# Kernel optimization log

Hardware: AMD Instinct MI355X
Metric: run time of the kernel (lower is better)

The kernel has to match this reference:

```python
import jax, jax.numpy as jnp
import numpy as np

N = 524288
H = 128
EPS = 1e-4
SYMP_N = 32  # min(N, 32)
# loss weights from init_kwargs
W_RECON, W_CONS, W_EVO, W_SYMP, W_GAUGE = 1.0, 10.0, 5.0, 0.1, 5.0


def _mlp(x, W1, b1, W2, b2, W3, b3):
    h = jnp.tanh(x @ W1 + b1)
    h = jnp.tanh(h @ W2 + b2)
    return h @ W3 + b3


def _encode(p, q, params):
    out = _mlp(jnp.stack([p, q], axis=-1), *params)  # [N,2]
    return out[:, 0], out[:, 1]


def _decode(P, Q, params):
    out = _mlp(jnp.stack([P, Q], axis=-1), *params)
    return out[:, 0], out[:, 1]


def setup_inputs() -> dict:
    key = jax.random.key(0)
    ks = jax.random.split(key, 24)
    f32 = jnp.float32

    def nrm(k, shape, scale=1.0):
        return (scale * jax.random.normal(k, shape, dtype=f32))

    inp = {
        'p0': nrm(ks[0], (N,)),
        'q0': nrm(ks[1], (N,)),
        'p1': nrm(ks[2], (N,)),
        'q1': nrm(ks[3], (N,)),
        'omega_values': jax.random.uniform(ks[4], (N,), dtype=f32, minval=0.5, maxval=2.0),
        'dt': jnp.asarray(0.05, dtype=f32),
        'P_true': nrm(ks[5], (N,)),
        'Q_true': nrm(ks[6], (N,)),
        # encoder params (2 -> H -> H -> 2), fan-in scaled init
        'enc_W1': nrm(ks[7], (2, H), 1.0 / np.sqrt(2.0)),
        'enc_b1': jnp.zeros((H,), f32),
        'enc_W2': nrm(ks[8], (H, H), 1.0 / np.sqrt(H)),
        'enc_b2': jnp.zeros((H,), f32),
        'enc_W3': nrm(ks[9], (H, 2), 1.0 / np.sqrt(H)),
        'enc_b3': jnp.zeros((2,), f32),
        # decoder params
        'dec_W1': nrm(ks[10], (2, H), 1.0 / np.sqrt(2.0)),
        'dec_b1': jnp.zeros((H,), f32),
        'dec_W2': nrm(ks[11], (H, H), 1.0 / np.sqrt(H)),
        'dec_b2': jnp.zeros((H,), f32),
        'dec_W3': nrm(ks[12], (H, 2), 1.0 / np.sqrt(H)),
        'dec_b3': jnp.zeros((2,), f32),
    }
    return inp


def _loss(p0, q0, p1, q1, omega_values, dt, P_true, Q_true, enc, dec):
    P0, Q0 = _encode(p0, q0, enc)
    P1, Q1 = _encode(p1, q1, enc)
    p0_recon, q0_recon = _decode(P0, Q0, dec)

    recon_loss = jnp.mean((p0 - p0_recon) ** 2 + (q0 - q0_recon) ** 2)
    conservation_loss = jnp.mean((P0 - P1) ** 2)
    evolution_loss = jnp.mean(1.0 - jnp.cos((Q1 - Q0) - omega_values * dt))

    # symplectic loss: batched central finite differences over first 32 samples
    pi, qi = p0[:SYMP_N], q0[:SYMP_N]
    pp = jnp.concatenate([pi + EPS, pi - EPS, pi, pi])          # [4*32]
    qq = jnp.concatenate([qi, qi, qi + EPS, qi - EPS])
    P, Q = _encode(pp, qq, enc)
    P_pp, P_pm, P_qp, P_qm = jnp.split(P, 4)
    Q_pp, Q_pm, Q_qp, Q_qm = jnp.split(Q, 4)
    inv2e = 1.0 / (2.0 * EPS)
    dP_dp = (P_pp - P_pm) * inv2e
    dP_dq = (P_qp - P_qm) * inv2e
    dQ_dp = (Q_pp - Q_pm) * inv2e
    dQ_dq = (Q_qp - Q_qm) * inv2e
    pb = dP_dq * dQ_dp - dP_dp * dQ_dq
    symplectic_loss = jnp.mean((jnp.abs(pb) - 1.0) ** 2)

    gauge_loss = jnp.mean((P0 - P_true) ** 2) + jnp.mean(1.0 - jnp.cos(Q0 - Q_true))

    total = (W_RECON * recon_loss + W_CONS * conservation_loss
             + W_EVO * evolution_loss + W_SYMP * symplectic_loss
             + W_GAUGE * gauge_loss)
    return jnp.stack([total, recon_loss, conservation_loss,
                      evolution_loss, symplectic_loss, gauge_loss])


def reference(p0, q0, p1, q1, omega_values, dt, P_true, Q_true,
              enc_W1, enc_b1, enc_W2, enc_b2, enc_W3, enc_b3,
              dec_W1, dec_b1, dec_W2, dec_b2, dec_W3, dec_b3):
    enc = (enc_W1, enc_b1, enc_W2, enc_b2, enc_W3, enc_b3)
    dec = (dec_W1, dec_b1, dec_W2, dec_b2, dec_W3, dec_b3)
    return _loss(p0, q0, p1, q1, omega_values, dt, P_true, Q_true, enc, dec)
```

## Files before the change

### kernel.cpp

```cpp
#include <hip/hip_runtime.h>
#include <stdint.h>
#include <math.h>


constexpr float EPS_FD = 1e-4f;
constexpr int NBLK = 256;

typedef float f32x4 __attribute__((ext_vector_type(4)));
typedef short s16x8 __attribute__((ext_vector_type(8)));

__device__ __forceinline__ float tanh_fast(float x) {
  float e = __builtin_amdgcn_exp2f(x * 2.8853900817779268f);
  return 1.0f - 2.0f * __builtin_amdgcn_rcpf(e + 1.0f);
}
__device__ __forceinline__ float cos_fast(float x) {
  return __builtin_amdgcn_cosf(x * 0.15915494309189535f);
}
__device__ __forceinline__ unsigned bf16rne(float f) {
  union { float f; unsigned u; } v; v.f = f;
  return (v.u + 0x7FFFu + ((v.u >> 16) & 1u)) >> 16;
}
__device__ __forceinline__ unsigned pack2rne(float a, float b) {
  return bf16rne(a) | (bf16rne(b) << 16);
}
__device__ __forceinline__ unsigned packbf(float lo, float hi) {
  union { float f; unsigned u; } a, b; a.f = lo; b.f = hi;
  return __builtin_amdgcn_perm(b.u + 0x8000u, a.u + 0x8000u, 0x07060302u);
}

__global__ void setup_kernel(const float* __restrict__ encW2,
                             const float* __restrict__ decW2,
                             unsigned* __restrict__ frag,
                             const float* __restrict__ p0, const float* __restrict__ q0,
                             const float* __restrict__ W1, const float* __restrict__ b1,
                             const float* __restrict__ W2, const float* __restrict__ b2,
                             const float* __restrict__ W3, const float* __restrict__ b3,
                             float* __restrict__ PQ,
                             float* __restrict__ acc5, unsigned* __restrict__ counter)
{
  int tid = threadIdx.x;
  if (blockIdx.x < 64) {
    if (blockIdx.x == 0 && tid < 6) {
      if (tid < 5) acc5[tid] = 0.f; else *counter = 0u;
    }
    int id = blockIdx.x * 256 + tid;
    const float* W = (id < 8192) ? encW2 : decW2;
    int l = id & 8191;
    int jj   = l & 3;
    int lane = (l >> 2) & 63;
    int f    = l >> 8;
    int s = f >> 3, t = f & 7;
    int quad = lane >> 4, nn = lane & 15;
    int k   = 32 * s + quad * 8 + 2 * jj;
    int col = 16 * t + nn;
    frag[id] = pack2rne(W[k * 128 + col], W[(k + 1) * 128 + col]);
  } else {
    int half = tid >> 7;
    int tt   = tid & 127;
    int row  = (blockIdx.x - 64) * 2 + half;
    int m = row & 31, c = row >> 5;
    float p = p0[m], q = q0[m];
    if (c == 0) p += EPS_FD; else if (c == 1) p -= EPS_FD;
    else if (c == 2) q += EPS_FD; else q -= EPS_FD;

    __shared__ float h1[2][128];
    h1[half][tt] = tanhf(fmaf(p, W1[tt], fmaf(q, W1[128 + tt], b1[tt])));
    __syncthreads();
    float a = b2[tt];
    for (int k = 0; k < 128; k++) a = fmaf(h1[half][k], W2[k * 128 + tt], a);
    float hh = tanhf(a);
    float cP = hh * W3[2 * tt];
    float cQ = hh * W3[2 * tt + 1];
#pragma unroll
    for (int mm = 1; mm < 64; mm <<= 1) {
      cP += __shfl_xor(cP, mm, 64);
      cQ += __shfl_xor(cQ, mm, 64);
    }
    __shared__ float rr[4][2];
    int wv = tid >> 6, ln = tid & 63;
    if (ln == 0) { rr[wv][0] = cP; rr[wv][1] = cQ; }
    __syncthreads();
    if (tt == 0) {
      PQ[2 * row]     = rr[2 * half][0] + rr[2 * half + 1][0] + b3[0];
      PQ[2 * row + 1] = rr[2 * half][1] + rr[2 * half + 1][1] + b3[1];
    }
  }
}

template<bool SCAT, bool EPI_LDS>
__device__ __forceinline__ void mlp_pass(
    float pe, float qe, unsigned* hrow, const uint4* Bf,
    float w100, float w101, float w110, float w111, float b10, float b11,
    const float (&rb2)[8], const float (&rw3P)[8], const float (&rw3Q)[8],
    const float* epi,
    int lane, int quad, int l15, float b3P, float b3Q,
    float& vP, float& vQ)
{
#pragma unroll
  for (int ee = 0; ee < 16; ee++) {
    int src = SCAT ? (16 * (ee >> 2) + (ee & 3)) : ee;
    float p = __shfl(pe, src, 64);
    float q = __shfl(qe, src, 64);
    float a0 = tanh_fast(fmaf(p, w100, fmaf(q, w110, b10)));
    float a1 = tanh_fast(fmaf(p, w101, fmaf(q, w111, b11)));
    hrow[ee * 68 + lane] = packbf(a0, a1);
  }
  __builtin_amdgcn_wave_barrier();

  s16x8 A[4];
#pragma unroll
  for (int s = 0; s < 4; s++) {
    uint4 u = *reinterpret_cast<const uint4*>(&hrow[l15 * 68 + 16 * s + 4 * quad]);
    A[s] = *reinterpret_cast<s16x8*>(&u);
  }
  __builtin_amdgcn_wave_barrier();

  float b2v[8];
#pragma unroll
  for (int t = 0; t < 8; t++) b2v[t] = EPI_LDS ? epi[16 * t + l15] : rb2[t];

  f32x4 acc[8];
#pragma unroll
  for (int t = 0; t < 8; t++) {
    f32x4 z = {b2v[t], b2v[t], b2v[t], b2v[t]};
    acc[t] = z;
  }
#pragma unroll
  for (int s = 0; s < 4; s++) {
#pragma unroll
    for (int t = 0; t < 8; t++) {
      uint4 bu = Bf[(s * 8 + t) * 64 + lane];
      s16x8 Bv = *reinterpret_cast<s16x8*>(&bu);
      acc[t] = __builtin_amdgcn_mfma_f32_16x16x32_bf16(A[s], Bv, acc[t], 0, 0, 0);
    }
  }

  float w3Pv[8], w3Qv[8];
#pragma unroll
  for (int t = 0; t < 8; t++) {
    w3Pv[t] = EPI_LDS ? epi[128 + 16 * t + l15] : rw3P[t];
    w3Qv[t] = EPI_LDS ? epi[256 + 16 * t + l15] : rw3Q[t];
  }

  float sP[4] = {0, 0, 0, 0}, sQ[4] = {0, 0, 0, 0};
#pragma unroll
  for (int t = 0; t < 8; t++) {
#pragma unroll
    for (int r = 0; r < 4; r++) {
      float h = tanh_fast(acc[t][r]);
      sP[r] = fmaf(h, w3Pv[t], sP[r]);
      sQ[r] = fmaf(h, w3Qv[t], sQ[r]);
    }
  }
#pragma unroll
  for (int m = 1; m < 16; m <<= 1) {
#pragma unroll
    for (int r = 0; r < 4; r++) {
      sP[r] += __shfl_xor(sP[r], m, 64);
      sQ[r] += __shfl_xor(sQ[r], m, 64);
    }
  }
  vP = ((l15 == 0) ? sP[0] : (l15 == 1) ? sP[1] : (l15 == 2) ? sP[2] : sP[3]) + b3P;
  vQ = ((l15 == 0) ? sQ[0] : (l15 == 1) ? sQ[1] : (l15 == 2) ? sQ[2] : sQ[3]) + b3Q;
}

__global__ __launch_bounds__(1024, 4) void mlp_all(
    const float* __restrict__ p0, const float* __restrict__ q0,
    const float* __restrict__ p1, const float* __restrict__ q1,
    const uint4* __restrict__ w2frag,
    const float* __restrict__ eW1, const float* __restrict__ eb1,
    const float* __restrict__ eb2, const float* __restrict__ eW3,
    const float* __restrict__ eb3,
    const float* __restrict__ dW1, const float* __restrict__ db1,
    const float* __restrict__ db2, const float* __restrict__ dW3,
    const float* __restrict__ db3,
    const float* __restrict__ omega, const float* __restrict__ Pt,
    const float* __restrict__ Qt, const float* __restrict__ dtp,
    float* __restrict__ acc5, unsigned* __restrict__ counter,
    const float* __restrict__ PQ, float* __restrict__ out, int n)
{
  __shared__ uint4 BfE[2048];
  __shared__ uint4 BfD[2048];
  __shared__ unsigned h1s[16][16 * 68 + 4];
  __shared__ float decEpi[384];
  __shared__ float red[16][5];
  __shared__ unsigned lastflag;

  int tid = threadIdx.x;
  for (int i = tid; i < 2048; i += 1024) {
    BfE[i] = w2frag[i];
    BfD[i] = w2frag[2048 + i];
  }
  if (tid < 128) {
    decEpi[tid]       = db2[tid];
    decEpi[128 + tid] = dW3[2 * tid];
    decEpi[256 + tid] = dW3[2 * tid + 1];
  }

  int wave = tid >> 6, lane = tid & 63;
  int quad = lane >> 4, l15 = lane & 15;

  float ew100 = eW1[2 * lane],       ew101 = eW1[2 * lane + 1];
  float ew110 = eW1[128 + 2 * lane], ew111 = eW1[128 + 2 * lane + 1];
  float eb10 = eb1[2 * lane], eb11 = eb1[2 * lane + 1];
  float dw100 = dW1[2 * lane],       dw101 = dW1[2 * lane + 1];
  float dw110 = dW1[128 + 2 * lane], dw111 = dW1[128 + 2 * lane + 1];
  float db10 = db1[2 * lane], db11 = db1[2 * lane + 1];
  float eb2v[8], ew3P[8], ew3Q[8];
#pragma unroll
  for (int t = 0; t < 8; t++) {
    eb2v[t] = eb2[16 * t + l15];
    ew3P[t] = eW3[(16 * t + l15) * 2];
    ew3Q[t] = eW3[(16 * t + l15) * 2 + 1];
  }
  float eb3P = eb3[0], eb3Q = eb3[1];
  float db3P = db3[0], db3Q = db3[1];
  float dt = dtp[0];
  float s0 = 0.f, s1 = 0.f, s2 = 0.f, s3 = 0.f, s4 = 0.f;
  __syncthreads();

  int nwaves = gridDim.x * 16;
  int gwave  = blockIdx.x * 16 + wave;
  int ntiles = (n + 15) >> 4;
  unsigned* hrow = &h1s[wave][0];

  for (int tile = gwave; tile < ntiles; tile += nwaves) {
    int base = tile * 16;
    int e = base + l15; if (e >= n) e = n - 1;
    float p0e = p0[e], q0e = q0[e];
    float p1e = p1[e], q1e = q1[e];
    int o = base + quad * 4 + l15;
    int o16 = base + quad * 4 + (l15 & 3);
    if (o16 >= n) o16 = n - 1;
    float Lom = omega[o16], LPt = Pt[o16], LQt = Qt[o16];
    float Lp0 = p0[o16],    Lq0 = q0[o16];

    float P0v, Q0v, P1v, Q1v, RPv, RQv;
    mlp_pass<false, false>(p0e, q0e, hrow, BfE,
                           ew100, ew101, ew110, ew111, eb10, eb11,
                           eb2v, ew3P, ew3Q, decEpi,
                           lane, quad, l15, eb3P, eb3Q, P0v, Q0v);
    mlp_pass<false, false>(p1e, q1e, hrow, BfE,
                           ew100, ew101, ew110, ew111, eb10, eb11,
                           eb2v, ew3P, ew3Q, decEpi,
                           lane, quad, l15, eb3P, eb3Q, P1v, Q1v);
    mlp_pass<true, true>(P0v, Q0v, hrow, BfD,
                         dw100, dw101, dw110, dw111, db10, db11,
                         eb2v, ew3P, ew3Q, decEpi,
                         lane, quad, l15, db3P, db3Q, RPv, RQv);

    if (l15 < 4 && o < n) {
      float dp = Lp0 - RPv, dq = Lq0 - RQv;
      s0 += dp * dp + dq * dq;
      float d1 = P0v - P1v; s1 += d1 * d1;
      s2 += 1.0f - cos_fast(Q1v - Q0v - Lom * dt);
      float g = P0v - LPt; s3 += g * g;
      s4 += 1.0f - cos_fast(Q0v - LQt);
    }
  }

#pragma unroll
  for (int m = 1; m < 64; m <<= 1) {
    s0 += __shfl_xor(s0, m, 64);
    s1 += __shfl_xor(s1, m, 64);
    s2 += __shfl_xor(s2, m, 64);
    s3 += __shfl_xor(s3, m, 64);
    s4 += __shfl_xor(s4, m, 64);
  }
  if (lane == 0) {
    red[wave][0] = s0; red[wave][1] = s1; red[wave][2] = s2;
    red[wave][3] = s3; red[wave][4] = s4;
  }
  __syncthreads();
  if (tid == 0) {
#pragma unroll
    for (int i = 0; i < 5; i++) {
      float v = 0.f;
#pragma unroll
      for (int w = 0; w < 16; w++) v += red[w][i];
      atomicAdd(&acc5[i], v);
    }
    __threadfence();
    unsigned prev = atomicAdd(counter, 1u);
    lastflag = (prev == gridDim.x - 1) ? 1u : 0u;
  }
  __syncthreads();
  if (lastflag) {
    __threadfence();
    if (tid < 64) {
      float v = 0.f;
      if (tid < 32) {
        float Ppp = PQ[2 * tid],          Qpp = PQ[2 * tid + 1];
        float Ppm = PQ[2 * (32 + tid)],   Qpm = PQ[2 * (32 + tid) + 1];
        float Pqp = PQ[2 * (64 + tid)],   Qqp = PQ[2 * (64 + tid) + 1];
        float Pqm = PQ[2 * (96 + tid)],   Qqm = PQ[2 * (96 + tid) + 1];
        float inv2e = 1.0f / (2.0f * EPS_FD);
        float dPdp = (Ppp - Ppm) * inv2e, dPdq = (Pqp - Pqm) * inv2e;
        float dQdp = (Qpp - Qpm) * inv2e, dQdq = (Qqp - Qqm) * inv2e;
        float pb = dPdq * dQdp - dPdp * dQdq;
        float d = fabsf(pb) - 1.0f;
        v = d * d;
      }
#pragma unroll
      for (int m = 1; m < 64; m <<= 1) v += __shfl_xor(v, m, 64);
      if (tid == 0) {
        float inv_n = 1.0f / (float)n;
        float recon = atomicAdd(&acc5[0], 0.f) * inv_n;
        float cons  = atomicAdd(&acc5[1], 0.f) * inv_n;
        float evo   = atomicAdd(&acc5[2], 0.f) * inv_n;
        float gauge = (atomicAdd(&acc5[3], 0.f) + atomicAdd(&acc5[4], 0.f)) * inv_n;
        float symp  = v * (1.0f / 32.0f);
        float total = recon + 10.0f * cons + 5.0f * evo + 0.1f * symp + 5.0f * gauge;
        out[0] = total; out[1] = recon; out[2] = cons;
        out[3] = evo;   out[4] = symp;  out[5] = gauge;
      }
    }
  }
}

extern "C" void kernel_launch(void* const* d_in, const int* in_sizes, int n_in,
                              void* d_out, int out_size, void* d_ws, size_t ws_size,
                              hipStream_t stream)
{
  const float* p0    = (const float*)d_in[0];
  const float* q0    = (const float*)d_in[1];
  const float* p1    = (const float*)d_in[2];
  const float* q1    = (const float*)d_in[3];
  const float* omega = (const float*)d_in[4];
  const float* dtp   = (const float*)d_in[5];
  const float* Pt    = (const float*)d_in[6];
  const float* Qt    = (const float*)d_in[7];
  const float* encW1 = (const float*)d_in[8];
  const float* encb1 = (const float*)d_in[9];
  const float* encW2 = (const float*)d_in[10];
  const float* encb2 = (const float*)d_in[11];
  const float* encW3 = (const float*)d_in[12];
  const float* encb3 = (const float*)d_in[13];
  const float* decW1 = (const float*)d_in[14];
  const float* decb1 = (const float*)d_in[15];
  const float* decW2 = (const float*)d_in[16];
  const float* decb2 = (const float*)d_in[17];
  const float* decW3 = (const float*)d_in[18];
  const float* decb3 = (const float*)d_in[19];

  int n = in_sizes[0];
  char* ws = (char*)d_ws;
  unsigned* frag = (unsigned*)ws;
  float* PQ   = (float*)(ws + 65536);
  float* acc5 = PQ + 256;
  unsigned* counter = (unsigned*)(acc5 + 8);

  setup_kernel<<<128, 256, 0, stream>>>(encW2, decW2, frag,
                                        p0, q0, encW1, encb1, encW2, encb2,
                                        encW3, encb3, PQ, acc5, counter);

  mlp_all<<<NBLK, 1024, 0, stream>>>(
      p0, q0, p1, q1, (const uint4*)frag,
      encW1, encb1, encb2, encW3, encb3,
      decW1, decb1, decb2, decW3, decb3,
      omega, Pt, Qt, dtp,
      acc5, counter, PQ, (float*)d_out, n);
}
```

Measured before the change: 293.0 us.

## Restructure launch: pack W2 fragments in-kernel, move symplectic FD and finalize to tail kernel

Removes the separate setup kernel: each main block now converts encoder/decoder W2 into bf16 MFMA fragments directly in LDS, and encoder epilogue weights move from registers to LDS. The last-block atomic counter finalization is replaced by a single-block tail kernel that computes the 32-sample finite-difference symplectic loss and the final output, plus a memset for the accumulators. The aim is to cut the serial setup stage and the counter handshake. In exchange every block redundantly reads and packs 2x64KB of weights, and the small tail kernel runs after the main one, adding its own latency.

```diff
diff --git a/kernel.cpp b/kernel.cpp
--- a/kernel.cpp
+++ b/kernel.cpp
@@ -28,73 +28,11 @@
   return __builtin_amdgcn_perm(b.u + 0x8000u, a.u + 0x8000u, 0x07060302u);
 }
 
-__global__ void setup_kernel(const float* __restrict__ encW2,
-                             const float* __restrict__ decW2,
-                             unsigned* __restrict__ frag,
-                             const float* __restrict__ p0, const float* __restrict__ q0,
-                             const float* __restrict__ W1, const float* __restrict__ b1,
-                             const float* __restrict__ W2, const float* __restrict__ b2,
-                             const float* __restrict__ W3, const float* __restrict__ b3,
-                             float* __restrict__ PQ,
-                             float* __restrict__ acc5, unsigned* __restrict__ counter)
-{
-  int tid = threadIdx.x;
-  if (blockIdx.x < 64) {
-    if (blockIdx.x == 0 && tid < 6) {
-      if (tid < 5) acc5[tid] = 0.f; else *counter = 0u;
-    }
-    int id = blockIdx.x * 256 + tid;
-    const float* W = (id < 8192) ? encW2 : decW2;
-    int l = id & 8191;
-    int jj   = l & 3;
-    int lane = (l >> 2) & 63;
-    int f    = l >> 8;
-    int s = f >> 3, t = f & 7;
-    int quad = lane >> 4, nn = lane & 15;
-    int k   = 32 * s + quad * 8 + 2 * jj;
-    int col = 16 * t + nn;
-    frag[id] = pack2rne(W[k * 128 + col], W[(k + 1) * 128 + col]);
-  } else {
-    int half = tid >> 7;
-    int tt   = tid & 127;
-    int row  = (blockIdx.x - 64) * 2 + half;
-    int m = row & 31, c = row >> 5;
-    float p = p0[m], q = q0[m];
-    if (c == 0) p += EPS_FD; else if (c == 1) p -= EPS_FD;
-    else if (c == 2) q += EPS_FD; else q -= EPS_FD;
-
-    __shared__ float h1[2][128];
-    h1[half][tt] = tanhf(fmaf(p, W1[tt], fmaf(q, W1[128 + tt], b1[tt])));
-    __syncthreads();
-    float a = b2[tt];
-    for (int k = 0; k < 128; k++) a = fmaf(h1[half][k], W2[k * 128 + tt], a);
-    float hh = tanhf(a);
-    float cP = hh * W3[2 * tt];
-    float cQ = hh * W3[2 * tt + 1];
-#pragma unroll
-    for (int mm = 1; mm < 64; mm <<= 1) {
-      cP += __shfl_xor(cP, mm, 64);
-      cQ += __shfl_xor(cQ, mm, 64);
-    }
-    __shared__ float rr[4][2];
-    int wv = tid >> 6, ln = tid & 63;
-    if (ln == 0) { rr[wv][0] = cP; rr[wv][1] = cQ; }
-    __syncthreads();
-    if (tt == 0) {
-      PQ[2 * row]     = rr[2 * half][0] + rr[2 * half + 1][0] + b3[0];
-      PQ[2 * row + 1] = rr[2 * half][1] + rr[2 * half + 1][1] + b3[1];
-    }
-  }
-}
-
-template<bool SCAT, bool EPI_LDS>
+template<bool SCAT>
 __device__ __forceinline__ void mlp_pass(
-    float pe, float qe, unsigned* hrow, const uint4* Bf,
+    float pe, float qe, unsigned* hrow, const uint4* Bf, const float* epi,
     float w100, float w101, float w110, float w111, float b10, float b11,
-    const float (&rb2)[8], const float (&rw3P)[8], const float (&rw3Q)[8],
-    const float* epi,
-    int lane, int quad, int l15, float b3P, float b3Q,
-    float& vP, float& vQ)
+    int lane, int quad, int l15, float& vP, float& vQ)
 {
 #pragma unroll
   for (int ee = 0; ee < 16; ee++) {
@@ -115,14 +53,11 @@
   }
   __builtin_amdgcn_wave_barrier();
 
-  float b2v[8];
-#pragma unroll
-  for (int t = 0; t < 8; t++) b2v[t] = EPI_LDS ? epi[16 * t + l15] : rb2[t];
-
   f32x4 acc[8];
 #pragma unroll
   for (int t = 0; t < 8; t++) {
-    f32x4 z = {b2v[t], b2v[t], b2v[t], b2v[t]};
+    float b2v = epi[16 * t + l15];
+    f32x4 z = {b2v, b2v, b2v, b2v};
     acc[t] = z;
   }
 #pragma unroll
@@ -135,21 +70,16 @@
     }
   }
 
-  float w3Pv[8], w3Qv[8];
+  float sP[4] = {0, 0, 0, 0}, sQ[4] = {0, 0, 0, 0};
 #pragma unroll
   for (int t = 0; t < 8; t++) {
-    w3Pv[t] = EPI_LDS ? epi[128 + 16 * t + l15] : rw3P[t];
-    w3Qv[t] = EPI_LDS ? epi[256 + 16 * t + l15] : rw3Q[t];
-  }
-
-  float sP[4] = {0, 0, 0, 0}, sQ[4] = {0, 0, 0, 0};
-#pragma unroll
-  for (int t = 0; t < 8; t++) {
+    float w3Pv = epi[128 + 16 * t + l15];
+    float w3Qv = epi[256 + 16 * t + l15];
 #pragma unroll
     for (int r = 0; r < 4; r++) {
       float h = tanh_fast(acc[t][r]);
-      sP[r] = fmaf(h, w3Pv[t], sP[r]);
-      sQ[r] = fmaf(h, w3Qv[t], sQ[r]);
+      sP[r] = fmaf(h, w3Pv, sP[r]);
+      sQ[r] = fmaf(h, w3Qv, sQ[r]);
     }
   }
 #pragma unroll
@@ -160,41 +90,50 @@
       sQ[r] += __shfl_xor(sQ[r], m, 64);
     }
   }
-  vP = ((l15 == 0) ? sP[0] : (l15 == 1) ? sP[1] : (l15 == 2) ? sP[2] : sP[3]) + b3P;
-  vQ = ((l15 == 0) ? sQ[0] : (l15 == 1) ? sQ[1] : (l15 == 2) ? sQ[2] : sQ[3]) + b3Q;
-}
-
-__global__ __launch_bounds__(1024, 4) void mlp_all(
+  vP = (l15 == 0) ? sP[0] : (l15 == 1) ? sP[1] : (l15 == 2) ? sP[2] : sP[3];
+  vQ = (l15 == 0) ? sQ[0] : (l15 == 1) ? sQ[1] : (l15 == 2) ? sQ[2] : sQ[3];
+}
+
+__global__ __launch_bounds__(1024, 1) void mlp_main(
     const float* __restrict__ p0, const float* __restrict__ q0,
     const float* __restrict__ p1, const float* __restrict__ q1,
-    const uint4* __restrict__ w2frag,
     const float* __restrict__ eW1, const float* __restrict__ eb1,
-    const float* __restrict__ eb2, const float* __restrict__ eW3,
-    const float* __restrict__ eb3,
+    const float* __restrict__ eW2, const float* __restrict__ eb2,
+    const float* __restrict__ eW3, const float* __restrict__ eb3,
     const float* __restrict__ dW1, const float* __restrict__ db1,
-    const float* __restrict__ db2, const float* __restrict__ dW3,
-    const float* __restrict__ db3,
+    const float* __restrict__ dW2, const float* __restrict__ db2,
+    const float* __restrict__ dW3, const float* __restrict__ db3,
     const float* __restrict__ omega, const float* __restrict__ Pt,
     const float* __restrict__ Qt, const float* __restrict__ dtp,
-    float* __restrict__ acc5, unsigned* __restrict__ counter,
-    const float* __restrict__ PQ, float* __restrict__ out, int n)
+    float* __restrict__ acc5, int n)
 {
   __shared__ uint4 BfE[2048];
   __shared__ uint4 BfD[2048];
   __shared__ unsigned h1s[16][16 * 68 + 4];
+  __shared__ float encEpi[384];
   __shared__ float decEpi[384];
   __shared__ float red[16][5];
-  __shared__ unsigned lastflag;
 
   int tid = threadIdx.x;
-  for (int i = tid; i < 2048; i += 1024) {
-    BfE[i] = w2frag[i];
-    BfD[i] = w2frag[2048 + i];
+#pragma unroll
+  for (int it = 0; it < 8; it++) {
+    int id = tid + it * 1024;
+    int jj = id & 3, ln = (id >> 2) & 63, f = id >> 8;
+    int s = f >> 3, t = f & 7;
+    int k   = 32 * s + 8 * (ln >> 4) + 2 * jj;
+    int col = 16 * t + (ln & 15);
+    ((unsigned*)BfE)[id] = pack2rne(eW2[k * 128 + col], eW2[(k + 1) * 128 + col]);
+    ((unsigned*)BfD)[id] = pack2rne(dW2[k * 128 + col], dW2[(k + 1) * 128 + col]);
   }
   if (tid < 128) {
-    decEpi[tid]       = db2[tid];
-    decEpi[128 + tid] = dW3[2 * tid];
-    decEpi[256 + tid] = dW3[2 * tid + 1];
+    encEpi[tid]       = eb2[tid];
+    encEpi[128 + tid] = eW3[2 * tid];
+    encEpi[256 + tid] = eW3[2 * tid + 1];
+  } else if (tid < 256) {
+    int u = tid - 128;
+    decEpi[u]       = db2[u];
+    decEpi[128 + u] = dW3[2 * u];
+    decEpi[256 + u] = dW3[2 * u + 1];
   }
 
   int wave = tid >> 6, lane = tid & 63;
@@ -206,13 +145,6 @@
   float dw100 = dW1[2 * lane],       dw101 = dW1[2 * lane + 1];
   float dw110 = dW1[128 + 2 * lane], dw111 = dW1[128 + 2 * lane + 1];
   float db10 = db1[2 * lane], db11 = db1[2 * lane + 1];
-  float eb2v[8], ew3P[8], ew3Q[8];
-#pragma unroll
-  for (int t = 0; t < 8; t++) {
-    eb2v[t] = eb2[16 * t + l15];
-    ew3P[t] = eW3[(16 * t + l15) * 2];
-    ew3Q[t] = eW3[(16 * t + l15) * 2 + 1];
-  }
   float eb3P = eb3[0], eb3Q = eb3[1];
   float db3P = db3[0], db3Q = db3[1];
   float dt = dtp[0];
@@ -236,18 +168,18 @@
     float Lp0 = p0[o16],    Lq0 = q0[o16];
 
     float P0v, Q0v, P1v, Q1v, RPv, RQv;
-    mlp_pass<false, false>(p0e, q0e, hrow, BfE,
-                           ew100, ew101, ew110, ew111, eb10, eb11,
-                           eb2v, ew3P, ew3Q, decEpi,
-                           lane, quad, l15, eb3P, eb3Q, P0v, Q0v);
-    mlp_pass<false, false>(p1e, q1e, hrow, BfE,
-                           ew100, ew101, ew110, ew111, eb10, eb11,
-                           eb2v, ew3P, ew3Q, decEpi,
-                           lane, quad, l15, eb3P, eb3Q, P1v, Q1v);
-    mlp_pass<true, true>(P0v, Q0v, hrow, BfD,
-                         dw100, dw101, dw110, dw111, db10, db11,
-                         eb2v, ew3P, ew3Q, decEpi,
-                         lane, quad, l15, db3P, db3Q, RPv, RQv);
+    mlp_pass<false>(p0e, q0e, hrow, BfE, encEpi,
+                    ew100, ew101, ew110, ew111, eb10, eb11,
+                    lane, quad, l15, P0v, Q0v);
+    P0v += eb3P; Q0v += eb3Q;
+    mlp_pass<false>(p1e, q1e, hrow, BfE, encEpi,
+                    ew100, ew101, ew110, ew111, eb10, eb11,
+                    lane, quad, l15, P1v, Q1v);
+    P1v += eb3P; Q1v += eb3Q;
+    mlp_pass<true>(P0v, Q0v, hrow, BfD, decEpi,
+                   dw100, dw101, dw110, dw111, db10, db11,
+                   lane, quad, l15, RPv, RQv);
+    RPv += db3P; RQv += db3Q;
 
     if (l15 < 4 && o < n) {
       float dp = Lp0 - RPv, dq = Lq0 - RQv;
@@ -272,48 +204,86 @@
     red[wave][3] = s3; red[wave][4] = s4;
   }
   __syncthreads();
-  if (tid == 0) {
-#pragma unroll
-    for (int i = 0; i < 5; i++) {
-      float v = 0.f;
-#pragma unroll
-      for (int w = 0; w < 16; w++) v += red[w][i];
-      atomicAdd(&acc5[i], v);
-    }
-    __threadfence();
-    unsigned prev = atomicAdd(counter, 1u);
-    lastflag = (prev == gridDim.x - 1) ? 1u : 0u;
-  }
-  __syncthreads();
-  if (lastflag) {
-    __threadfence();
-    if (tid < 64) {
-      float v = 0.f;
-      if (tid < 32) {
-        float Ppp = PQ[2 * tid],          Qpp = PQ[2 * tid + 1];
-        float Ppm = PQ[2 * (32 + tid)],   Qpm = PQ[2 * (32 + tid) + 1];
-        float Pqp = PQ[2 * (64 + tid)],   Qqp = PQ[2 * (64 + tid) + 1];
-        float Pqm = PQ[2 * (96 + tid)],   Qqm = PQ[2 * (96 + tid) + 1];
-        float inv2e = 1.0f / (2.0f * EPS_FD);
-        float dPdp = (Ppp - Ppm) * inv2e, dPdq = (Pqp - Pqm) * inv2e;
-        float dQdp = (Qpp - Qpm) * inv2e, dQdq = (Qqp - Qqm) * inv2e;
-        float pb = dPdq * dQdp - dPdp * dQdq;
-        float d = fabsf(pb) - 1.0f;
-        v = d * d;
-      }
-#pragma unroll
-      for (int m = 1; m < 64; m <<= 1) v += __shfl_xor(v, m, 64);
-      if (tid == 0) {
-        float inv_n = 1.0f / (float)n;
-        float recon = atomicAdd(&acc5[0], 0.f) * inv_n;
-        float cons  = atomicAdd(&acc5[1], 0.f) * inv_n;
-        float evo   = atomicAdd(&acc5[2], 0.f) * inv_n;
-        float gauge = (atomicAdd(&acc5[3], 0.f) + atomicAdd(&acc5[4], 0.f)) * inv_n;
-        float symp  = v * (1.0f / 32.0f);
-        float total = recon + 10.0f * cons + 5.0f * evo + 0.1f * symp + 5.0f * gauge;
-        out[0] = total; out[1] = recon; out[2] = cons;
-        out[3] = evo;   out[4] = symp;  out[5] = gauge;
-      }
+  if (tid < 5) {
+    float v = 0.f;
+#pragma unroll
+    for (int w = 0; w < 16; w++) v += red[w][tid];
+    atomicAdd(&acc5[tid], v);
+  }
+}
+
+__global__ __launch_bounds__(1024) void symp_final(
+    const float* __restrict__ p0, const float* __restrict__ q0,
+    const float* __restrict__ W1, const float* __restrict__ b1,
+    const float* __restrict__ W2, const float* __restrict__ b2,
+    const float* __restrict__ W3, const float* __restrict__ b3,
+    const float* __restrict__ acc5, float* __restrict__ out, int n)
+{
+  __shared__ float h1L[8][128];
+  __shared__ float PQL[128][2];
+  __shared__ float wred[16][2];
+
+  int tid = threadIdx.x;
+  int tt = tid & 127, rgrp = tid >> 7;
+  float W1a = W1[tt], W1b = W1[128 + tt], b1v = b1[tt];
+  float b2v = b2[tt], w3a = W3[2 * tt], w3b = W3[2 * tt + 1];
+  float b3P = b3[0], b3Q = b3[1];
+
+  for (int batch = 0; batch < 16; batch++) {
+    int row = batch * 8 + rgrp;
+    int m = row & 31, c = row >> 5;
+    float p = p0[m], q = q0[m];
+    p += (c == 0) ? EPS_FD : (c == 1) ? -EPS_FD : 0.f;
+    q += (c == 2) ? EPS_FD : (c == 3) ? -EPS_FD : 0.f;
+    h1L[rgrp][tt] = tanhf(fmaf(p, W1a, fmaf(q, W1b, b1v)));
+    __syncthreads();
+    float a = b2v;
+#pragma unroll 8
+    for (int k = 0; k < 128; k++)
+      a = fmaf(h1L[rgrp][k], W2[k * 128 + tt], a);
+    float h2 = tanhf(a);
+    float cP = h2 * w3a, cQ = h2 * w3b;
+#pragma unroll
+    for (int mm = 1; mm < 64; mm <<= 1) {
+      cP += __shfl_xor(cP, mm, 64);
+      cQ += __shfl_xor(cQ, mm, 64);
+    }
+    int wv = tid >> 6;
+    if ((tid & 63) == 0) { wred[wv][0] = cP; wred[wv][1] = cQ; }
+    __syncthreads();
+    if (tt == 0) {
+      PQL[row][0] = wred[2 * rgrp][0] + wred[2 * rgrp + 1][0] + b3P;
+      PQL[row][1] = wred[2 * rgrp][1] + wred[2 * rgrp + 1][1] + b3Q;
+    }
+    __syncthreads();
+  }
+
+  if (tid < 64) {
+    float v = 0.f;
+    if (tid < 32) {
+      float Ppp = PQL[tid][0],      Qpp = PQL[tid][1];
+      float Ppm = PQL[32 + tid][0], Qpm = PQL[32 + tid][1];
+      float Pqp = PQL[64 + tid][0], Qqp = PQL[64 + tid][1];
+      float Pqm = PQL[96 + tid][0], Qqm = PQL[96 + tid][1];
+      float inv2e = 1.0f / (2.0f * EPS_FD);
+      float dPdp = (Ppp - Ppm) * inv2e, dPdq = (Pqp - Pqm) * inv2e;
+      float dQdp = (Qpp - Qpm) * inv2e, dQdq = (Qqp - Qqm) * inv2e;
+      float pb = dPdq * dQdp - dPdp * dQdq;
+      float d = fabsf(pb) - 1.0f;
+      v = d * d;
+    }
+#pragma unroll
+    for (int m = 1; m < 64; m <<= 1) v += __shfl_xor(v, m, 64);
+    if (tid == 0) {
+      float inv_n = 1.0f / (float)n;
+      float recon = acc5[0] * inv_n;
+      float cons  = acc5[1] * inv_n;
+      float evo   = acc5[2] * inv_n;
+      float gauge = (acc5[3] + acc5[4]) * inv_n;
+      float symp  = v * (1.0f / 32.0f);
+      float total = recon + 10.0f * cons + 5.0f * evo + 0.1f * symp + 5.0f * gauge;
+      out[0] = total; out[1] = recon; out[2] = cons;
+      out[3] = evo;   out[4] = symp;  out[5] = gauge;
     }
   }
 }
@@ -344,20 +314,17 @@
   const float* decb3 = (const float*)d_in[19];
 
   int n = in_sizes[0];
-  char* ws = (char*)d_ws;
-  unsigned* frag = (unsigned*)ws;
-  float* PQ   = (float*)(ws + 65536);
-  float* acc5 = PQ + 256;
-  unsigned* counter = (unsigned*)(acc5 + 8);
-
-  setup_kernel<<<128, 256, 0, stream>>>(encW2, decW2, frag,
-                                        p0, q0, encW1, encb1, encW2, encb2,
-                                        encW3, encb3, PQ, acc5, counter);
-
-  mlp_all<<<NBLK, 1024, 0, stream>>>(
-      p0, q0, p1, q1, (const uint4*)frag,
-      encW1, encb1, encb2, encW3, encb3,
-      decW1, decb1, decb2, decW3, decb3,
-      omega, Pt, Qt, dtp,
-      acc5, counter, PQ, (float*)d_out, n);
-}
+  float* acc5 = (float*)d_ws;
+
+  hipMemsetAsync(acc5, 0, 8 * sizeof(float), stream);
+
+  mlp_main<<<NBLK, 1024, 0, stream>>>(
+      p0, q0, p1, q1,
+      encW1, encb1, encW2, encb2, encW3, encb3,
+      decW1, decb1, decW2, decb2, decW3, decb3,
+      omega, Pt, Qt, dtp, acc5, n);
+
+  symp_final<<<1, 1024, 0, stream>>>(
+      p0, q0, encW1, encb1, encW2, encb2, encW3, encb3,
+      acc5, (float*)d_out, n);
+}
```

Result: slower. 338.0 us (+15.4%).
